# Kernel tuning notes

Hardware: AMD Instinct MI355X
Metric: run time of the kernel (lower is better)

The kernel has to match this reference:

```python
import jax, jax.numpy as jnp
import numpy as np
from jax import lax

B, C_IN, C_OUT, H, W, K = 32, 128, 256, 56, 56, 3
STRIDE, PAD = 1, 1
LAMBDA_C, LAMBDA_A = 0.0, 1.0  # adaptive_weights=False defaults


def setup_inputs() -> dict:
    key = jax.random.key(0)
    k1, k2, k3 = jax.random.split(key, 3)
    x = jax.random.normal(k1, (B, C_IN, H, W), dtype=jnp.float32)
    weight = jax.random.normal(k2, (C_OUT, C_IN, K, K), dtype=jnp.float32) * 0.05
    bias = jax.random.normal(k3, (C_OUT,), dtype=jnp.float32) * 0.05
    return {"x": x, "weight": weight, "bias": bias}


def reference(x, weight, bias):
    # For each k x k patch X and kernel slice Kc (per in-channel):
    #   sum(X@Kc) = sum_{a,c} X[a,c] * rowsum(Kc)[c]   (depends on patch column index)
    #   sum(Kc@X) = sum_{c,b} X[c,b] * colsum(Kc)[c]   (depends on patch row index)
    # So lambda_c*(XK-KX).sum() + lambda_a*(XK+KX).sum() summed over in-channels is
    # exactly a conv2d with the effective kernel below.
    krow = weight.sum(axis=3)  # [O, I, k]  rowsum: sum over last kernel axis
    kcol = weight.sum(axis=2)  # [O, I, k]  colsum: sum over first kernel axis
    # W_eff[o,i,r,s] = (la+lc)*krow[o,i,s] + (la-lc)*kcol[o,i,r]
    w_eff = (LAMBDA_A + LAMBDA_C) * krow[:, :, None, :] \
          + (LAMBDA_A - LAMBDA_C) * kcol[:, :, :, None]
    y = lax.conv_general_dilated(
        x, w_eff,
        window_strides=(STRIDE, STRIDE),
        padding=[(PAD, PAD), (PAD, PAD)],
        dimension_numbers=("NCHW", "OIHW", "NCHW"),
    )
    return y + bias[None, :, None, None]
```

## Files before the change

kernel.cpp:

```cpp
#include <hip/hip_runtime.h>
#include <stdint.h>

typedef unsigned short u16;
typedef short short8 __attribute__((ext_vector_type(8)));
typedef float floatx4 __attribute__((ext_vector_type(4)));

#define B_N 32
#define CI  128
#define CO  256
#define HH  56
#define WW  56
#define HP  58
#define WP  58

static const size_t XP_OFF = 590080;

__device__ __forceinline__ float bf2f(u16 u) {
  union { uint32_t i; float f; } c; c.i = ((uint32_t)u) << 16; return c.f;
}
__device__ __forceinline__ u16 f2bf(float f) {
  union { float f; uint32_t i; } c; c.f = f;
  uint32_t u = c.i;
  u += 0x7fffu + ((u >> 16) & 1u);
  return (u16)(u >> 16);
}
__device__ __forceinline__ uint32_t pack2bf(float a, float b) {
  return (uint32_t)f2bf(a) | ((uint32_t)f2bf(b) << 16);
}

__device__ __forceinline__ bool detect_bf16(const void* __restrict__ bias) {
  int lane = threadIdx.x & 63;
  float a = fabsf(bf2f(((const u16*)bias)[lane]));
  bool plausible = (a >= 1e-5f) && (a <= 0.5f);
  unsigned long long m = __ballot(plausible);
  return __popcll(m) >= 50;
}

__global__ __launch_bounds__(256) void k_prep(const void* __restrict__ xsrc,
                                              const void* __restrict__ wsrc,
                                              u16* __restrict__ xp,
                                              u16* __restrict__ wb,
                                              const void* __restrict__ bias) {
  const int hp = blockIdx.x, b = blockIdx.y, tid = threadIdx.x;
  if (hp == HP) {
    const bool isbf = detect_bf16(bias);
#pragma unroll 1
    for (int sub = 0; sub < 4; ++sub) {
      int t = (b * 4 + sub) * 256 + tid;
      float v[9];
      if (isbf) {
        const u16* p = (const u16*)wsrc + (size_t)t * 9;
#pragma unroll
        for (int j = 0; j < 9; ++j) v[j] = bf2f(p[j]);
      } else {
        const float* p = (const float*)wsrc + (size_t)t * 9;
#pragma unroll
        for (int j = 0; j < 9; ++j) v[j] = p[j];
      }
      float rowsum[3] = { v[0]+v[1]+v[2], v[3]+v[4]+v[5], v[6]+v[7]+v[8] };
      float colsum[3] = { v[0]+v[3]+v[6], v[1]+v[4]+v[7], v[2]+v[5]+v[8] };
      const int o = t >> 7, i = t & 127;
      const int osub = o >> 4, lo = o & 15;
      const int ic = i >> 5, q = (i >> 3) & 3, j = i & 7;
#pragma unroll
      for (int r = 0; r < 3; ++r)
#pragma unroll
        for (int s = 0; s < 3; ++s) {
          int k = (r * 3 + s) * 4 + ic;
          wb[((size_t)(k * 16 + osub) * 64 + q * 16 + lo) * 8 + j] = f2bf(rowsum[s] + colsum[r]);
        }
    }
    return;
  }
  __shared__ uint32_t tile32[CI * 29];
  u16* dst = xp + (size_t)(b * HP + hp) * (16 * WP * 8);
  if (hp == 0 || hp == HP - 1) {
    int4 z = {0, 0, 0, 0};
    for (int c = tid; c < 928; c += 256) *(int4*)(dst + c * 8) = z;
    return;
  }
  const bool isbf = detect_bf16(bias);
  const int h = hp - 1;
  if (isbf) {
    const uint32_t* xr = (const uint32_t*)xsrc;
    for (int c = tid; c < CI * 28; c += 256) {
      int i = c / 28, wp = c - i * 28;
      tile32[i * 29 + wp] = xr[((size_t)(b * CI + i) * HH + h) * 28 + wp];
    }
  } else {
    const float4* xr = (const float4*)xsrc;
    for (int c = tid; c < CI * 14; c += 256) {
      int i = c / 14, f4 = c - i * 14;
      float4 v = xr[((size_t)(b * CI + i) * HH + h) * 14 + f4];
      tile32[i * 29 + 2 * f4]     = pack2bf(v.x, v.y);
      tile32[i * 29 + 2 * f4 + 1] = pack2bf(v.z, v.w);
    }
  }
  __syncthreads();
  const u16* t16 = (const u16*)tile32;
  uint32_t* dw = (uint32_t*)dst;
  for (int c = tid; c < 16 * 56 * 4; c += 256) {
    int g = c / 224, rem = c - g * 224, w = rem >> 2, jj = rem & 3;
    int i0 = g * 8 + jj * 2;
    uint32_t lo16 = t16[i0 * 58 + w], hi16 = t16[(i0 + 1) * 58 + w];
    dw[(g * 58 + (w + 1)) * 4 + jj] = lo16 | (hi16 << 16);
  }
  if (tid < 128) {
    int g = tid >> 3, k = tid & 7, wb_ = (k >> 2) * 57, jj = k & 3;
    dw[(g * 58 + wb_) * 4 + jj] = 0;
  }
}

#define ALOAD(DST, K)                                                            \
  {                                                                              \
    const u16* ap = wb + ((size_t)((K)*16 + osubbase) << 9) + lane * 8;          \
    DST##0 = *(const short8*)ap;                                                 \
    DST##1 = *(const short8*)(ap + 512);                                         \
    DST##2 = *(const short8*)(ap + 1024);                                        \
    DST##3 = *(const short8*)(ap + 1536);                                        \
  }
#define BLOAD(DST, K)                                                            \
  {                                                                              \
    int rs_ = (K) >> 2, ic_ = (K)&3;                                             \
    int r_ = (rs_ * 86) >> 8, s_ = rs_ - r_ * 3;                                 \
    const u16* bp = Bs + (((r_ * 16 + ic_ * 4 + quad) * 58) + lo + s_) * 8;      \
    DST##0 = *(const short8*)bp;                                                 \
    DST##1 = *(const short8*)(bp + 128);                                         \
    DST##2 = *(const short8*)(bp + 256);                                         \
    DST##3 = *(const short8*)(bp + 384);                                         \
  }
#define MSTEP(A, Bf)                                                                   \
  {                                                                                    \
    short8 am_[4] = {A##0, A##1, A##2, A##3};                                          \
    short8 bn_[4] = {Bf##0, Bf##1, Bf##2, Bf##3};                                      \
    _Pragma("unroll") for (int m = 0; m < 4; ++m)                                      \
        _Pragma("unroll") for (int n = 0; n < 4; ++n) acc[m][n] =                      \
            __builtin_amdgcn_mfma_f32_16x16x32_bf16(am_[m], bn_[n], acc[m][n], 0, 0, 0); \
  }

__global__ __launch_bounds__(256, 3) void k_gemm(const u16* __restrict__ wb,
                                                 const u16* __restrict__ xp,
                                                 const void* __restrict__ bias,
                                                 void* __restrict__ outv) {
  __shared__ u16 Bs[3 * 16 * 58 * 8 + 128];
  const int p = blockIdx.x, b = blockIdx.y;
  const int tid = threadIdx.x;
  const int wv = tid >> 6, lane = tid & 63;
  const int lo = lane & 15, quad = lane >> 4;
  const int wm = wv;
  const int osubbase = wm * 4;

  {
    const u16* src = xp + (size_t)(b * HP + p) * (16 * WP * 8);
    for (int c = tid; c < 2784; c += 256)
      *(int4*)(Bs + (size_t)c * 8) = *(const int4*)(src + (size_t)c * 8);
  }
  __syncthreads();

  floatx4 acc[4][4];
#pragma unroll
  for (int m = 0; m < 4; ++m)
#pragma unroll
    for (int n = 0; n < 4; ++n) acc[m][n] = (floatx4){0.f, 0.f, 0.f, 0.f};

  short8 a00, a01, a02, a03, a10, a11, a12, a13;
  short8 b00, b01, b02, b03, b10, b11, b12, b13;
  ALOAD(a0, 0); BLOAD(b0, 0);
#pragma unroll 1
  for (int k = 0; k < 36; k += 2) {
    ALOAD(a1, k + 1); BLOAD(b1, k + 1);
    MSTEP(a0, b0);
    if (k + 2 < 36) { ALOAD(a0, k + 2); BLOAD(b0, k + 2); }
    MSTEP(a1, b1);
  }

  const bool isbf = detect_bf16(bias);
  if (isbf) {
    u16* out = (u16*)outv;
    const u16* bs = (const u16*)bias;
#pragma unroll
    for (int m = 0; m < 4; ++m)
#pragma unroll
      for (int v = 0; v < 4; ++v) {
        const int o = wm * 64 + m * 16 + quad * 4 + v;
        const float bv = bf2f(bs[o]);
        size_t base = ((size_t)(b * CO + o) * HH + p) * WW;
#pragma unroll
        for (int n = 0; n < 4; ++n) {
          const int q = n * 16 + lo;
          if (q < WW) out[base + q] = f2bf(acc[m][n][v] + bv);
        }
      }
  } else {
    float* out = (float*)outv;
    const float* bs = (const float*)bias;
#pragma unroll
    for (int m = 0; m < 4; ++m)
#pragma unroll
      for (int v = 0; v < 4; ++v) {
        const int o = wm * 64 + m * 16 + quad * 4 + v;
        const float bv = bs[o];
        size_t base = ((size_t)(b * CO + o) * HH + p) * WW;
#pragma unroll
        for (int n = 0; n < 4; ++n) {
          const int q = n * 16 + lo;
          if (q < WW) out[base + q] = acc[m][n][v] + bv;
        }
      }
  }
}

extern "C" void kernel_launch(void* const* d_in, const int* in_sizes, int n_in,
                              void* d_out, int out_size, void* d_ws, size_t ws_size,
                              hipStream_t stream) {
  const void* x    = d_in[0];
  const void* w    = d_in[1];
  const void* bias = d_in[2];
  uint8_t* ws = (uint8_t*)d_ws;
  u16* wb = (u16*)ws;
  u16* xp = (u16*)(ws + XP_OFF);

  k_prep<<<dim3(HP + 1, B_N), 256, 0, stream>>>(x, w, xp, wb, bias);
  k_gemm<<<dim3(HH, B_N), 256, 0, stream>>>(wb, xp, bias, d_out);
}
```

Before: 213.2 us.

## Compute two output rows per block to reuse weight fragments

Each GEMM block now computes two adjacent output rows, loading four padded input rows into shared memory and doubling the N tile to 8 MFMA columns per wave. This halves the number of weight-fragment global loads per output and halves the grid size. The shared-memory row stride is padded (59 instead of 58 entries per group) to reduce LDS bank conflicts. In exchange the accumulator registers double, and launch bounds drop occupancy from 3 to 2 blocks per CU.

```diff
diff --git a/kernel.cpp b/kernel.cpp
--- a/kernel.cpp
+++ b/kernel.cpp
@@ -111,67 +111,72 @@
   }
 }
 
-#define ALOAD(DST, K)                                                            \
-  {                                                                              \
-    const u16* ap = wb + ((size_t)((K)*16 + osubbase) << 9) + lane * 8;          \
-    DST##0 = *(const short8*)ap;                                                 \
-    DST##1 = *(const short8*)(ap + 512);                                         \
-    DST##2 = *(const short8*)(ap + 1024);                                        \
-    DST##3 = *(const short8*)(ap + 1536);                                        \
-  }
-#define BLOAD(DST, K)                                                            \
-  {                                                                              \
-    int rs_ = (K) >> 2, ic_ = (K)&3;                                             \
-    int r_ = (rs_ * 86) >> 8, s_ = rs_ - r_ * 3;                                 \
-    const u16* bp = Bs + (((r_ * 16 + ic_ * 4 + quad) * 58) + lo + s_) * 8;      \
-    DST##0 = *(const short8*)bp;                                                 \
-    DST##1 = *(const short8*)(bp + 128);                                         \
-    DST##2 = *(const short8*)(bp + 256);                                         \
-    DST##3 = *(const short8*)(bp + 384);                                         \
-  }
-#define MSTEP(A, Bf)                                                                   \
-  {                                                                                    \
-    short8 am_[4] = {A##0, A##1, A##2, A##3};                                          \
-    short8 bn_[4] = {Bf##0, Bf##1, Bf##2, Bf##3};                                      \
-    _Pragma("unroll") for (int m = 0; m < 4; ++m)                                      \
-        _Pragma("unroll") for (int n = 0; n < 4; ++n) acc[m][n] =                      \
-            __builtin_amdgcn_mfma_f32_16x16x32_bf16(am_[m], bn_[n], acc[m][n], 0, 0, 0); \
-  }
-
-__global__ __launch_bounds__(256, 3) void k_gemm(const u16* __restrict__ wb,
+#define GSTRIDE 472
+#define RSTRIDE (16 * 472)
+
+#define ALOAD(BUF, K)                                                       \
+  {                                                                         \
+    const u16* ap = wb + ((size_t)((K)*16 + osubbase) << 9) + lane * 8;     \
+    af[BUF][0] = *(const short8*)ap;                                        \
+    af[BUF][1] = *(const short8*)(ap + 512);                                \
+    af[BUF][2] = *(const short8*)(ap + 1024);                               \
+    af[BUF][3] = *(const short8*)(ap + 1536);                               \
+  }
+#define BLOAD(BUF, K)                                                       \
+  {                                                                         \
+    int rs_ = (K) >> 2, ic_ = (K)&3;                                        \
+    int r_ = (rs_ * 86) >> 8, s_ = rs_ - r_ * 3;                            \
+    const u16* bp = Bs + ((r_ * 16 + ic_ * 4 + quad) * GSTRIDE) + (lo + s_) * 8; \
+    bfr[BUF][0] = *(const short8*)bp;                                       \
+    bfr[BUF][1] = *(const short8*)(bp + 128);                               \
+    bfr[BUF][2] = *(const short8*)(bp + 256);                               \
+    bfr[BUF][3] = *(const short8*)(bp + 384);                               \
+    bfr[BUF][4] = *(const short8*)(bp + RSTRIDE);                           \
+    bfr[BUF][5] = *(const short8*)(bp + RSTRIDE + 128);                     \
+    bfr[BUF][6] = *(const short8*)(bp + RSTRIDE + 256);                     \
+    bfr[BUF][7] = *(const short8*)(bp + RSTRIDE + 384);                     \
+  }
+#define MSTEP(BUF)                                                          \
+  _Pragma("unroll") for (int m = 0; m < 4; ++m)                             \
+      _Pragma("unroll") for (int n = 0; n < 8; ++n) acc[m][n] =             \
+          __builtin_amdgcn_mfma_f32_16x16x32_bf16(af[BUF][m], bfr[BUF][n],  \
+                                                  acc[m][n], 0, 0, 0);
+
+__global__ __launch_bounds__(256, 2) void k_gemm(const u16* __restrict__ wb,
                                                  const u16* __restrict__ xp,
                                                  const void* __restrict__ bias,
                                                  void* __restrict__ outv) {
-  __shared__ u16 Bs[3 * 16 * 58 * 8 + 128];
-  const int p = blockIdx.x, b = blockIdx.y;
+  __shared__ u16 Bs[4 * RSTRIDE + 64];
+  const int p0 = 2 * blockIdx.x, b = blockIdx.y;
   const int tid = threadIdx.x;
   const int wv = tid >> 6, lane = tid & 63;
   const int lo = lane & 15, quad = lane >> 4;
-  const int wm = wv;
-  const int osubbase = wm * 4;
+  const int osubbase = wv * 4;
 
   {
-    const u16* src = xp + (size_t)(b * HP + p) * (16 * WP * 8);
-    for (int c = tid; c < 2784; c += 256)
-      *(int4*)(Bs + (size_t)c * 8) = *(const int4*)(src + (size_t)c * 8);
+    const u16* src = xp + (size_t)(b * HP + p0) * (16 * WP * 8);
+    for (int c = tid; c < 3712; c += 256) {
+      int row = c / 928, rem = c - row * 928;
+      int g = rem / 58, w = rem - g * 58;
+      *(int4*)(Bs + (size_t)((row * 16 + g) * 59 + w) * 8) = *(const int4*)(src + (size_t)c * 8);
+    }
   }
   __syncthreads();
 
-  floatx4 acc[4][4];
+  floatx4 acc[4][8];
 #pragma unroll
   for (int m = 0; m < 4; ++m)
 #pragma unroll
-    for (int n = 0; n < 4; ++n) acc[m][n] = (floatx4){0.f, 0.f, 0.f, 0.f};
-
-  short8 a00, a01, a02, a03, a10, a11, a12, a13;
-  short8 b00, b01, b02, b03, b10, b11, b12, b13;
-  ALOAD(a0, 0); BLOAD(b0, 0);
+    for (int n = 0; n < 8; ++n) acc[m][n] = (floatx4){0.f, 0.f, 0.f, 0.f};
+
+  short8 af[2][4], bfr[2][8];
+  ALOAD(0, 0); BLOAD(0, 0);
 #pragma unroll 1
   for (int k = 0; k < 36; k += 2) {
-    ALOAD(a1, k + 1); BLOAD(b1, k + 1);
-    MSTEP(a0, b0);
-    if (k + 2 < 36) { ALOAD(a0, k + 2); BLOAD(b0, k + 2); }
-    MSTEP(a1, b1);
+    ALOAD(1, k + 1); BLOAD(1, k + 1);
+    MSTEP(0);
+    if (k + 2 < 36) { ALOAD(0, k + 2); BLOAD(0, k + 2); }
+    MSTEP(1);
   }
 
   const bool isbf = detect_bf16(bias);
@@ -182,13 +187,13 @@
     for (int m = 0; m < 4; ++m)
 #pragma unroll
       for (int v = 0; v < 4; ++v) {
-        const int o = wm * 64 + m * 16 + quad * 4 + v;
+        const int o = wv * 64 + m * 16 + quad * 4 + v;
         const float bv = bf2f(bs[o]);
-        size_t base = ((size_t)(b * CO + o) * HH + p) * WW;
-#pragma unroll
-        for (int n = 0; n < 4; ++n) {
-          const int q = n * 16 + lo;
-          if (q < WW) out[base + q] = f2bf(acc[m][n][v] + bv);
+        size_t base = ((size_t)(b * CO + o) * HH + p0) * WW;
+#pragma unroll
+        for (int n = 0; n < 8; ++n) {
+          const int q = (n & 3) * 16 + lo;
+          if (q < WW) out[base + (n >> 2) * WW + q] = f2bf(acc[m][n][v] + bv);
         }
       }
   } else {
@@ -198,13 +203,13 @@
     for (int m = 0; m < 4; ++m)
 #pragma unroll
       for (int v = 0; v < 4; ++v) {
-        const int o = wm * 64 + m * 16 + quad * 4 + v;
+        const int o = wv * 64 + m * 16 + quad * 4 + v;
         const float bv = bs[o];
-        size_t base = ((size_t)(b * CO + o) * HH + p) * WW;
-#pragma unroll
-        for (int n = 0; n < 4; ++n) {
-          const int q = n * 16 + lo;
-          if (q < WW) out[base + q] = acc[m][n][v] + bv;
+        size_t base = ((size_t)(b * CO + o) * HH + p0) * WW;
+#pragma unroll
+        for (int n = 0; n < 8; ++n) {
+          const int q = (n & 3) * 16 + lo;
+          if (q < WW) out[base + (n >> 2) * WW + q] = acc[m][n][v] + bv;
         }
       }
   }
@@ -221,5 +226,5 @@
   u16* xp = (u16*)(ws + XP_OFF);
 
   k_prep<<<dim3(HP + 1, B_N), 256, 0, stream>>>(x, w, xp, wb, bias);
-  k_gemm<<<dim3(HH, B_N), 256, 0, stream>>>(wb, xp, bias, d_out);
-}
+  k_gemm<<<dim3(HH / 2, B_N), 256, 0, stream>>>(wb, xp, bias, d_out);
+}
```

After: 202.3 us. 5.1% less time.
